# Kernel optimization log

Hardware: AMD Instinct MI355X
Metric: run time of the kernel (lower is better)

## Reference

```python
import jax, jax.numpy as jnp
import numpy as np

FLOW_ITERS = 8
DUAL_ITERS = 8
DUAL_STEP = 0.1
DUAL_MOM = 0.9
GRAPH_LAYERS = 2
BIG = 1e9


def _sparsemax(z, mask):
    # sparsemax along last axis; masked entries already hold -BIG, zeroed by mask after.
    V = z.shape[-1]
    zs = jnp.sort(z, axis=-1)[..., ::-1]
    cum = jnp.cumsum(zs, axis=-1)
    k = jnp.arange(1, V + 1, dtype=z.dtype)
    support = zs * k > (cum - 1.0)
    k_sel = jnp.sum(support.astype(jnp.int32), axis=-1, keepdims=True)
    tau = (jnp.take_along_axis(cum, k_sel - 1, axis=-1) - 1.0) / k_sel.astype(z.dtype)
    return jnp.maximum(z - tau, 0.0) * mask


def _min_cost_flow(props, demands):
    # iterative proportional flow routing: push relu(inflow - demand) along predicted proportions
    def body(flow, _):
        inflow = jnp.sum(flow, axis=1)[..., None]      # [B,V,1] inflow to each node
        adjusted = jax.nn.relu(inflow - demands)       # excess to re-route
        return props * adjusted, None                  # row i scaled by its excess
    flow0 = jnp.zeros_like(props)
    flow, _ = jax.lax.scan(body, flow0, None, length=FLOW_ITERS)
    return flow


def _dual_flow(dual_diff, adj):
    # Nesterov-momentum projected gradient on cost(x)=x^2 minus linear dual term, x>=0 on edges
    def body(carry, _):
        flow, acc = carry
        look = flow - DUAL_MOM * acc
        grad = 2.0 * look - dual_diff                  # d/dx x^2 - dual_diff
        acc = DUAL_MOM * acc + DUAL_STEP * grad
        flow = adj * jax.nn.relu(flow - acc)
        return (flow, acc), None
    z = jnp.zeros_like(dual_diff)
    (flow, _), _ = jax.lax.scan(body, (z, z), None, length=DUAL_ITERS)
    return flow


def setup_inputs():
    key = jax.random.key(0)
    ks = jax.random.split(key, 32)
    B, V, F, E, D, K, H = 8, 1200, 8, 16, 64, 2, 4
    node_features = jax.random.normal(ks[0], (B, V, F), dtype=jnp.float32)
    node_embeddings = jax.random.normal(ks[1], (B, V, E), dtype=jnp.float32)
    d = jax.random.normal(ks[2], (B, V, 1), dtype=jnp.float32)
    demands = d - jnp.mean(d, axis=1, keepdims=True)   # balanced supply/demand per graph
    eye = jnp.eye(V, dtype=jnp.float32)
    adj = (jax.random.uniform(ks[3], (B, V, V)) < (16.0 / V)).astype(jnp.float32) * (1.0 - eye)
    hop2 = jnp.clip(adj @ adj, 0.0, 1.0) * (1.0 - eye)
    neighborhoods = jnp.stack([adj, hop2], axis=0)     # [K,B,V,V] k-hop neighborhoods

    def dense(k, fin, fout):
        return (jax.random.normal(k, (fin, fout), dtype=jnp.float32) / np.sqrt(fin)).astype(jnp.float32)

    return dict(
        node_features=node_features, node_embeddings=node_embeddings,
        demands=demands, adj=adj, neighborhoods=neighborhoods,
        enc_w0=dense(ks[4], E + F, D), enc_b0=jnp.zeros((D,), jnp.float32),
        enc_w1=dense(ks[5], D, D), enc_b1=jnp.zeros((D,), jnp.float32),
        agg_w=(jax.random.normal(ks[6], (K, D, D)) / np.sqrt(D)).astype(jnp.float32),
        agg_b=jnp.zeros((K, D), jnp.float32),
        att_w=(jax.random.normal(ks[7], (H, D, D)) / np.sqrt(D)).astype(jnp.float32),
        att_b=jnp.zeros((H, D), jnp.float32),
        att_v=(jax.random.normal(ks[8], (H, D)) / np.sqrt(D)).astype(jnp.float32),
        gru_wu=dense(ks[9], 2 * D, D), gru_bu=jnp.zeros((D,), jnp.float32),
        gru_wr=dense(ks[10], 2 * D, D), gru_br=jnp.zeros((D,), jnp.float32),
        gru_wc=dense(ks[11], 2 * D, D), gru_bc=jnp.zeros((D,), jnp.float32),
        dec_w0=dense(ks[12], D, D), dec_b0=jnp.zeros((D,), jnp.float32),
        dec_w1=dense(ks[13], D, 1), dec_b1=jnp.zeros((1,), jnp.float32),
        dual_w0=dense(ks[14], D, D), dual_b0=jnp.zeros((D,), jnp.float32),
        dual_w1=dense(ks[15], D, 1), dual_b1=jnp.zeros((1,), jnp.float32),
    )


def reference(node_features, node_embeddings, demands, adj, neighborhoods,
              enc_w0, enc_b0, enc_w1, enc_b1, agg_w, agg_b, att_w, att_b, att_v,
              gru_wu, gru_bu, gru_wr, gru_br, gru_wc, gru_bc,
              dec_w0, dec_b0, dec_w1, dec_b1, dual_w0, dual_b0, dual_w1, dual_b1):
    H = att_w.shape[0]
    # node encoder MLP (tanh hidden, tanh final since activate_final=True)
    x = jnp.concatenate([node_embeddings, node_features], axis=-1)
    enc = jnp.tanh(jnp.tanh(x @ enc_w0 + enc_b0) @ enc_w1 + enc_b1)            # [B,V,D]

    deg = jnp.sum(neighborhoods, axis=-1, keepdims=True)
    nb_norm = neighborhoods / jnp.maximum(deg, 1.0)                            # [K,B,V,V]

    for _ in range(GRAPH_LAYERS):
        # per-hop neighborhood aggregation
        msg = jnp.einsum('kbuv,bvd->kbud', nb_norm, enc)
        agg = jnp.tanh(jnp.einsum('kbud,kde->kbue', msg, agg_w) + agg_b[:, None, None, :])
        # multi-head attention over the K hop levels
        proj = jnp.tanh(jnp.einsum('kbvd,hde->hkbve', agg, att_w) + att_b[:, None, None, None, :])
        scores = jnp.einsum('hkbve,he->hkbv', proj, att_v)
        attn = jax.nn.softmax(scores, axis=1)                                  # softmax over hops
        nxt = jnp.einsum('hkbv,kbvd->bvd', attn, agg) / H                      # mean over heads
        # GRU state update
        xs = jnp.concatenate([nxt, enc], axis=-1)
        u = jax.nn.sigmoid(xs @ gru_wu + gru_bu)
        r = jax.nn.sigmoid(xs @ gru_wr + gru_br)
        c = jnp.tanh(jnp.concatenate([nxt, r * enc], axis=-1) @ gru_wc + gru_bc)
        enc = u * enc + (1.0 - u) * c

    # primal: edge weights -> sparsemax -> min-cost-flow
    pred = (enc @ dec_w0 + dec_b0) @ dec_w1 + dec_b1                           # [B,V,1]
    pred_weights = adj * jnp.transpose(pred, (0, 2, 1))                        # [B,V,V]
    weights = -BIG * (1.0 - adj) + pred_weights
    flow_props = _sparsemax(weights, adj)
    flow = _min_cost_flow(flow_props, demands)
    flow_cost = jnp.sum(flow * flow, axis=(1, 2))                              # square cost

    # dual: potentials -> dual-diff -> dual flow solver
    dual = (enc @ dual_w0 + dual_b0) @ dual_w1 + dual_b1                       # [B,V,1]
    dual_diff = adj * (dual - jnp.transpose(dual, (0, 2, 1)))
    dflow = _dual_flow(dual_diff, adj)
    dual_demand = jnp.sum(dual * demands, axis=(1, 2))
    dual_cost = jnp.sum(dflow * dflow - dual_diff * dflow, axis=(1, 2)) - dual_demand

    return flow_cost - dual_cost                                               # duality-gap loss, [B]
```

## Files before the change

### kernel.cpp

```cpp
#include <hip/hip_runtime.h>

#define BB 8
#define VV 1200
#define DD 64
#define KH 2
#define NH 4
#define CAP 64
#define NB2CAP 384
#define NROW (BB*VV)
#define NKROW (KH*BB*VV)

__device__ __forceinline__ float wredsum(float v) {
#pragma unroll
  for (int o = 32; o > 0; o >>= 1) v += __shfl_xor(v, o, 64);
  return v;
}
__device__ __forceinline__ float gredsum(float v) {
#pragma unroll
  for (int o = 8; o > 0; o >>= 1) v += __shfl_xor(v, o, 64);
  return v;
}

__device__ __forceinline__ float tanh_f(float x) {
  float e = __expf(2.0f * x);
  return 1.0f - 2.0f / (e + 1.0f);
}
__device__ __forceinline__ float sigmoid_f(float x) { return 1.0f / (1.0f + __expf(-x)); }

__device__ __forceinline__ size_t nb_base(int row) {
  return (row < NROW) ? (size_t)row * CAP
                      : (size_t)NROW * CAP + (size_t)(row - NROW) * NB2CAP;
}

__global__ void __launch_bounds__(256) k_pre(
    const float* __restrict__ nb, int* __restrict__ nb_cols, int* __restrict__ nb_cnt,
    const float* __restrict__ emb, const float* __restrict__ feat,
    const float* __restrict__ w0, const float* __restrict__ b0,
    const float* __restrict__ w1, const float* __restrict__ b1,
    float* __restrict__ enc0,
    int* __restrict__ col_cnt, float* __restrict__ out, int out_size) {
  __shared__ float xT[8][25];
  __shared__ float hT[8][65];
  const int nbBlocks = NKROW / 4;
  const int encBlocks = NROW / 8;
  int bid = blockIdx.x;
  int tid = threadIdx.x;
  if (bid < nbBlocks) {
    int wid = tid >> 6, lane = tid & 63;
    int row = bid * 4 + wid;
    const float* nbrow = nb + (size_t)row * VV;
    size_t base = nb_base(row);
    int cap = (row < NROW) ? CAP : NB2CAP;
    unsigned long long ltmask = (lane == 0) ? 0ull : ((1ull << lane) - 1ull);
    int cnt = 0;
    for (int b0_ = 0; b0_ < VV; b0_ += 64) {
      int v = b0_ + lane;
      float val = (v < VV) ? nbrow[v] : 0.0f;
      unsigned long long mask = __ballot(val != 0.0f);
      int off = cnt + __popcll(mask & ltmask);
      if (val != 0.0f && off < cap) nb_cols[base + off] = v;
      cnt += __popcll(mask);
    }
    if (lane == 0) nb_cnt[row] = (cnt > cap) ? cap : cnt;
  } else if (bid < nbBlocks + encBlocks) {
    int tile0 = (bid - nbBlocks) * 8;
    if (tid < 128) { int i = tid >> 4, d = tid & 15; xT[i][d] = emb[(size_t)(tile0 + i) * 16 + d]; }
    else if (tid < 192) { int t = tid - 128; int i = t >> 3, d = t & 7; xT[i][16 + d] = feat[(size_t)(tile0 + i) * 8 + d]; }
    __syncthreads();
    int r = tid >> 5, cg = tid & 31;
    int c0 = cg * 2;
    float a0 = b0[c0], a1 = b0[c0 + 1];
#pragma unroll
    for (int kk = 0; kk < 24; ++kk) {
      float x = xT[r][kk];
      float2 w2 = *(const float2*)(w0 + kk * DD + c0);
      a0 = fmaf(x, w2.x, a0); a1 = fmaf(x, w2.y, a1);
    }
    hT[r][c0] = tanh_f(a0); hT[r][c0 + 1] = tanh_f(a1);
    __syncthreads();
    float g0 = b1[c0], g1 = b1[c0 + 1];
#pragma unroll 16
    for (int kk = 0; kk < DD; ++kk) {
      float x = hT[r][kk];
      float2 w2 = *(const float2*)(w1 + kk * DD + c0);
      g0 = fmaf(x, w2.x, g0); g1 = fmaf(x, w2.y, g1);
    }
    float2 o; o.x = tanh_f(g0); o.y = tanh_f(g1);
    *(float2*)(enc0 + (size_t)(tile0 + r) * DD + c0) = o;
  } else {
    for (int i = tid; i < NROW; i += 256) col_cnt[i] = 0;
    if (tid < out_size) out[tid] = 0.0f;
  }
}

__global__ void __launch_bounds__(256) k_gather(
    const int* __restrict__ nb_cols, const int* __restrict__ nb_cnt,
    const float* __restrict__ encIn, float* __restrict__ msg) {
  int w = threadIdx.x >> 6, lane = threadIdx.x & 63;
  int row = blockIdx.x * 4 + w;
  int k = (row >= NROW) ? 1 : 0;
  int bv = row - k * NROW;
  int b = bv / VV;
  const float4* enc4 = (const float4*)(encIn + (size_t)b * VV * DD);
  const int* cols = nb_cols + nb_base(row);
  int n = nb_cnt[row];
  int sub = lane >> 4, q = lane & 15;
  float ax = 0.0f, ay = 0.0f, az = 0.0f, aw = 0.0f;
  int j = 0;
  int cc0 = 0, cc1 = 0, cc2 = 0, cc3 = 0;
  if (j + 16 <= n) {
    cc0 = cols[j + sub]; cc1 = cols[j + 4 + sub];
    cc2 = cols[j + 8 + sub]; cc3 = cols[j + 12 + sub];
  }
  while (j + 16 <= n) {
    int nj = j + 16;
    int p0 = 0, p1 = 0, p2 = 0, p3 = 0;
    if (nj + 16 <= n) {
      p0 = cols[nj + sub]; p1 = cols[nj + 4 + sub];
      p2 = cols[nj + 8 + sub]; p3 = cols[nj + 12 + sub];
    }
    float4 v0 = enc4[(size_t)cc0 * 16 + q];
    float4 v1 = enc4[(size_t)cc1 * 16 + q];
    float4 v2 = enc4[(size_t)cc2 * 16 + q];
    float4 v3 = enc4[(size_t)cc3 * 16 + q];
    ax += (v0.x + v1.x) + (v2.x + v3.x);
    ay += (v0.y + v1.y) + (v2.y + v3.y);
    az += (v0.z + v1.z) + (v2.z + v3.z);
    aw += (v0.w + v1.w) + (v2.w + v3.w);
    cc0 = p0; cc1 = p1; cc2 = p2; cc3 = p3;
    j = nj;
  }
  for (; j < n; j += 4) {
    int idx = j + sub;
    if (idx < n) {
      float4 v = enc4[(size_t)cols[idx] * 16 + q];
      ax += v.x; ay += v.y; az += v.z; aw += v.w;
    }
  }
#pragma unroll
  for (int o = 16; o < 64; o <<= 1) {
    ax += __shfl_xor(ax, o, 64);
    ay += __shfl_xor(ay, o, 64);
    az += __shfl_xor(az, o, 64);
    aw += __shfl_xor(aw, o, 64);
  }
  if (lane < 16) {
    float inv = 1.0f / fmaxf((float)n, 1.0f);
    float4 r; r.x = ax * inv; r.y = ay * inv; r.z = az * inv; r.w = aw * inv;
    ((float4*)(msg + (size_t)row * DD))[q] = r;
  }
}

__global__ void __launch_bounds__(512) k_aggatt(
    const float* __restrict__ msg,
    const float* __restrict__ agg_w, const float* __restrict__ agg_b,
    const float* __restrict__ att_w, const float* __restrict__ att_b,
    const float* __restrict__ att_v,
    float* __restrict__ agg, float* __restrict__ scores) {
  __shared__ float M[64][65];
  __shared__ float G[64][65];
  int tid = threadIdx.x;
  int tile0 = blockIdx.x * 64;
  int k = (tile0 >= NROW) ? 1 : 0;
  int bv0 = tile0 - k * NROW;
  int rsub = tid >> 4, cg = tid & 15;
  int c0 = cg * 4;
  int r0 = rsub * 2;
#pragma unroll
  for (int rep = 0; rep < 2; ++rep) {
    int idx = rep * 512 + tid; int i = idx >> 4, d4 = idx & 15;
    float4 m4 = *(const float4*)(msg + (size_t)(tile0 + i) * DD + d4 * 4);
    M[i][d4 * 4] = m4.x; M[i][d4 * 4 + 1] = m4.y; M[i][d4 * 4 + 2] = m4.z; M[i][d4 * 4 + 3] = m4.w;
  }
  __syncthreads();
  const float* W = agg_w + (size_t)k * DD * DD;
  float acc[2][4];
#pragma unroll
  for (int i = 0; i < 2; ++i)
#pragma unroll
    for (int j = 0; j < 4; ++j) acc[i][j] = agg_b[k * DD + c0 + j];
#pragma unroll 4
  for (int kk = 0; kk < DD; ++kk) {
    float4 w4 = *(const float4*)(W + kk * DD + c0);
    float x0 = M[r0][kk], x1 = M[r0 + 1][kk];
    acc[0][0] = fmaf(x0, w4.x, acc[0][0]); acc[0][1] = fmaf(x0, w4.y, acc[0][1]);
    acc[0][2] = fmaf(x0, w4.z, acc[0][2]); acc[0][3] = fmaf(x0, w4.w, acc[0][3]);
    acc[1][0] = fmaf(x1, w4.x, acc[1][0]); acc[1][1] = fmaf(x1, w4.y, acc[1][1]);
    acc[1][2] = fmaf(x1, w4.z, acc[1][2]); acc[1][3] = fmaf(x1, w4.w, acc[1][3]);
  }
#pragma unroll
  for (int i = 0; i < 2; ++i) {
    float4 g4;
    g4.x = tanh_f(acc[i][0]); g4.y = tanh_f(acc[i][1]);
    g4.z = tanh_f(acc[i][2]); g4.w = tanh_f(acc[i][3]);
    G[r0 + i][c0] = g4.x; G[r0 + i][c0 + 1] = g4.y; G[r0 + i][c0 + 2] = g4.z; G[r0 + i][c0 + 3] = g4.w;
    *(float4*)(agg + (size_t)(tile0 + r0 + i) * DD + c0) = g4;
  }
  __syncthreads();
#pragma unroll
  for (int h = 0; h < NH; ++h) {
    const float* Wh = att_w + (size_t)h * DD * DD;
    float a2[2][4];
#pragma unroll
    for (int i = 0; i < 2; ++i)
#pragma unroll
      for (int j = 0; j < 4; ++j) a2[i][j] = att_b[h * DD + c0 + j];
#pragma unroll 4
    for (int kk = 0; kk < DD; ++kk) {
      float4 w4 = *(const float4*)(Wh + kk * DD + c0);
      float x0 = G[r0][kk], x1 = G[r0 + 1][kk];
      a2[0][0] = fmaf(x0, w4.x, a2[0][0]); a2[0][1] = fmaf(x0, w4.y, a2[0][1]);
      a2[0][2] = fmaf(x0, w4.z, a2[0][2]); a2[0][3] = fmaf(x0, w4.w, a2[0][3]);
      a2[1][0] = fmaf(x1, w4.x, a2[1][0]); a2[1][1] = fmaf(x1, w4.y, a2[1][1]);
      a2[1][2] = fmaf(x1, w4.z, a2[1][2]); a2[1][3] = fmaf(x1, w4.w, a2[1][3]);
    }
    float4 v4 = *(const float4*)(att_v + h * DD + c0);
#pragma unroll
    for (int i = 0; i < 2; ++i) {
      float p = tanh_f(a2[i][0]) * v4.x + tanh_f(a2[i][1]) * v4.y
              + tanh_f(a2[i][2]) * v4.z + tanh_f(a2[i][3]) * v4.w;
      p = gredsum(p);
      if (cg == 0) scores[(size_t)(h * KH + k) * NROW + bv0 + r0 + i] = p;
    }
  }
}

__global__ void __launch_bounds__(512) k_gru(
    const float* __restrict__ encIn, const float* __restrict__ agg,
    const float* __restrict__ scores,
    const float* __restrict__ wu, const float* __restrict__ bu,
    const float* __restrict__ wr, const float* __restrict__ br,
    const float* __restrict__ wc, const float* __restrict__ bc,
    float* __restrict__ encOut,
    int do_decode,
    const float* __restrict__ dw0, const float* __restrict__ db0,
    const float* __restrict__ dw1, const float* __restrict__ db1,
    const float* __restrict__ uw0, const float* __restrict__ ub0,
    const float* __restrict__ uw1, const float* __restrict__ ub1,
    float* __restrict__ pred, float* __restrict__ dualp) {
  __shared__ float X[64][129];
  __shared__ float EO[64][65];
  int tid = threadIdx.x;
  int tile0 = blockIdx.x * 64;
  int rsub = tid >> 4, cg = tid & 15;
  int c0 = cg * 4;
  int r0 = rsub * 2;
#pragma unroll
  for (int rep = 0; rep < 2; ++rep) {
    int idx = rep * 512 + tid; int i = idx >> 4, d4 = idx & 15;
    int row = tile0 + i;
    float W0 = 0.0f, W1 = 0.0f;
#pragma unroll
    for (int h = 0; h < NH; ++h) {
      float s0 = scores[(size_t)(h * KH + 0) * NROW + row];
      float s1 = scores[(size_t)(h * KH + 1) * NROW + row];
      float m = fmaxf(s0, s1);
      float e0 = __expf(s0 - m), e1 = __expf(s1 - m);
      float inv = 1.0f / (e0 + e1);
      W0 += e0 * inv; W1 += e1 * inv;
    }
    W0 *= 0.25f; W1 *= 0.25f;
    float4 e4 = *(const float4*)(encIn + (size_t)row * DD + d4 * 4);
    float4 a0 = *(const float4*)(agg + (size_t)row * DD + d4 * 4);
    float4 a1 = *(const float4*)(agg + (size_t)(NROW + row) * DD + d4 * 4);
    X[i][d4 * 4]     = W0 * a0.x + W1 * a1.x;
    X[i][d4 * 4 + 1] = W0 * a0.y + W1 * a1.y;
    X[i][d4 * 4 + 2] = W0 * a0.z + W1 * a1.z;
    X[i][d4 * 4 + 3] = W0 * a0.w + W1 * a1.w;
    X[i][64 + d4 * 4]     = e4.x;
    X[i][64 + d4 * 4 + 1] = e4.y;
    X[i][64 + d4 * 4 + 2] = e4.z;
    X[i][64 + d4 * 4 + 3] = e4.w;
  }
  __syncthreads();
  float au[2][4], ar[2][4];
#pragma unroll
  for (int i = 0; i < 2; ++i)
#pragma unroll
    for (int j = 0; j < 4; ++j) { au[i][j] = bu[c0 + j]; ar[i][j] = br[c0 + j]; }
#pragma unroll 4
  for (int kk = 0; kk < 2 * DD; ++kk) {
    float4 u4 = *(const float4*)(wu + kk * DD + c0);
    float4 r4 = *(const float4*)(wr + kk * DD + c0);
    float x0 = X[r0][kk], x1 = X[r0 + 1][kk];
    au[0][0] = fmaf(x0, u4.x, au[0][0]); au[0][1] = fmaf(x0, u4.y, au[0][1]);
    au[0][2] = fmaf(x0, u4.z, au[0][2]); au[0][3] = fmaf(x0, u4.w, au[0][3]);
    au[1][0] = fmaf(x1, u4.x, au[1][0]); au[1][1] = fmaf(x1, u4.y, au[1][1]);
    au[1][2] = fmaf(x1, u4.z, au[1][2]); au[1][3] = fmaf(x1, u4.w, au[1][3]);
    ar[0][0] = fmaf(x0, r4.x, ar[0][0]); ar[0][1] = fmaf(x0, r4.y, ar[0][1]);
    ar[0][2] = fmaf(x0, r4.z, ar[0][2]); ar[0][3] = fmaf(x0, r4.w, ar[0][3]);
    ar[1][0] = fmaf(x1, r4.x, ar[1][0]); ar[1][1] = fmaf(x1, r4.y, ar[1][1]);
    ar[1][2] = fmaf(x1, r4.z, ar[1][2]); ar[1][3] = fmaf(x1, r4.w, ar[1][3]);
  }
  float uu[2][4], encv[2][4];
#pragma unroll
  for (int i = 0; i < 2; ++i)
#pragma unroll
    for (int j = 0; j < 4; ++j) {
      uu[i][j] = sigmoid_f(au[i][j]);
      encv[i][j] = X[r0 + i][64 + c0 + j];
    }
  __syncthreads();
#pragma unroll
  for (int i = 0; i < 2; ++i)
#pragma unroll
    for (int j = 0; j < 4; ++j)
      X[r0 + i][64 + c0 + j] = encv[i][j] * sigmoid_f(ar[i][j]);
  __syncthreads();
  float ac[2][4];
#pragma unroll
  for (int i = 0; i < 2; ++i)
#pragma unroll
    for (int j = 0; j < 4; ++j) ac[i][j] = bc[c0 + j];
#pragma unroll 4
  for (int kk = 0; kk < 2 * DD; ++kk) {
    float4 c4 = *(const float4*)(wc + kk * DD + c0);
    float x0 = X[r0][kk], x1 = X[r0 + 1][kk];
    ac[0][0] = fmaf(x0, c4.x, ac[0][0]); ac[0][1] = fmaf(x0, c4.y, ac[0][1]);
    ac[0][2] = fmaf(x0, c4.z, ac[0][2]); ac[0][3] = fmaf(x0, c4.w, ac[0][3]);
    ac[1][0] = fmaf(x1, c4.x, ac[1][0]); ac[1][1] = fmaf(x1, c4.y, ac[1][1]);
    ac[1][2] = fmaf(x1, c4.z, ac[1][2]); ac[1][3] = fmaf(x1, c4.w, ac[1][3]);
  }
#pragma unroll
  for (int i = 0; i < 2; ++i) {
    float4 e4;
    e4.x = uu[i][0] * encv[i][0] + (1.0f - uu[i][0]) * tanh_f(ac[i][0]);
    e4.y = uu[i][1] * encv[i][1] + (1.0f - uu[i][1]) * tanh_f(ac[i][1]);
    e4.z = uu[i][2] * encv[i][2] + (1.0f - uu[i][2]) * tanh_f(ac[i][2]);
    e4.w = uu[i][3] * encv[i][3] + (1.0f - uu[i][3]) * tanh_f(ac[i][3]);
    *(float4*)(encOut + (size_t)(tile0 + r0 + i) * DD + c0) = e4;
    EO[r0 + i][c0] = e4.x; EO[r0 + i][c0 + 1] = e4.y;
    EO[r0 + i][c0 + 2] = e4.z; EO[r0 + i][c0 + 3] = e4.w;
  }
  if (do_decode) {
    __syncthreads();
    float hd[2][4], hq[2][4];
#pragma unroll
    for (int i = 0; i < 2; ++i)
#pragma unroll
      for (int j = 0; j < 4; ++j) { hd[i][j] = db0[c0 + j]; hq[i][j] = ub0[c0 + j]; }
#pragma unroll 4
    for (int kk = 0; kk < DD; ++kk) {
      float4 d4 = *(const float4*)(dw0 + kk * DD + c0);
      float4 q4 = *(const float4*)(uw0 + kk * DD + c0);
      float x0 = EO[r0][kk], x1 = EO[r0 + 1][kk];
      hd[0][0] = fmaf(x0, d4.x, hd[0][0]); hd[0][1] = fmaf(x0, d4.y, hd[0][1]);
      hd[0][2] = fmaf(x0, d4.z, hd[0][2]); hd[0][3] = fmaf(x0, d4.w, hd[0][3]);
      hd[1][0] = fmaf(x1, d4.x, hd[1][0]); hd[1][1] = fmaf(x1, d4.y, hd[1][1]);
      hd[1][2] = fmaf(x1, d4.z, hd[1][2]); hd[1][3] = fmaf(x1, d4.w, hd[1][3]);
      hq[0][0] = fmaf(x0, q4.x, hq[0][0]); hq[0][1] = fmaf(x0, q4.y, hq[0][1]);
      hq[0][2] = fmaf(x0, q4.z, hq[0][2]); hq[0][3] = fmaf(x0, q4.w, hq[0][3]);
      hq[1][0] = fmaf(x1, q4.x, hq[1][0]); hq[1][1] = fmaf(x1, q4.y, hq[1][1]);
      hq[1][2] = fmaf(x1, q4.z, hq[1][2]); hq[1][3] = fmaf(x1, q4.w, hq[1][3]);
    }
    float4 dv = *(const float4*)(dw1 + c0);
    float4 qv = *(const float4*)(uw1 + c0);
#pragma unroll
    for (int i = 0; i < 2; ++i) {
      float p = hd[i][0] * dv.x + hd[i][1] * dv.y + hd[i][2] * dv.z + hd[i][3] * dv.w;
      float q = hq[i][0] * qv.x + hq[i][1] * qv.y + hq[i][2] * qv.z + hq[i][3] * qv.w;
      p = gredsum(p);
      q = gredsum(q);
      if (cg == 0) {
        pred[tile0 + r0 + i] = p + db1[0];
        dualp[tile0 + r0 + i] = q + ub1[0];
      }
    }
  }
}

__global__ void __launch_bounds__(256) k_primal_dual(
    const int* __restrict__ nb_cols, const int* __restrict__ nb_cnt,
    const float* __restrict__ pred, const float* __restrict__ dualp,
    const float* __restrict__ dem,
    float* __restrict__ rowsum,
    int* __restrict__ col_cnt, int* __restrict__ col_rows, float* __restrict__ col_vals,
    float* __restrict__ out) {
  __shared__ float bacc[BB];
  if (threadIdx.x < BB) bacc[threadIdx.x] = 0.0f;
  __syncthreads();
  int w = threadIdx.x >> 6, lane = threadIdx.x & 63;
  int row = blockIdx.x * 4 + w;
  int b = row / VV;
  int n = nb_cnt[row];
  int c = (lane < n) ? nb_cols[(size_t)row * CAP + lane] : 0;
  const float* predB = pred + (size_t)b * VV;
  const float* dualB = dualp + (size_t)b * VV;
  float z = (lane < n) ? predB[c] : -1e30f;
  float tau = 0.0f;
  if (n > 0) {
    bool in = (lane < n);
    for (int it = 0; it < 64; ++it) {
      float s = wredsum(in ? z : 0.0f);
      int cnt = (int)__popcll(__ballot(in));
      tau = (s - 1.0f) / (float)cnt;
      bool nin = (z > tau);
      if (__ballot(nin) == __ballot(in)) break;
      in = nin;
    }
  }
  float pv = (lane < n) ? fmaxf(z - tau, 0.0f) : 0.0f;
  float s2 = wredsum(pv * pv);
  if (lane == 0) rowsum[row] = s2;
  if (pv > 0.0f) {
    int g = b * VV + c;
    int j = atomicAdd(&col_cnt[g], 1);
    if (j < CAP) {
      col_rows[(size_t)g * CAP + j] = row - b * VV;
      col_vals[(size_t)g * CAP + j] = pv;
    }
  }
  float du = dualp[row];
  float es = 0.0f;
  if (lane < n) {
    float dd = du - dualB[c];
    float f = 0.0f, acm = 0.0f;
#pragma unroll
    for (int t = 0; t < 8; ++t) {
      float look = f - 0.9f * acm;
      float grad = 2.0f * look - dd;
      acm = 0.9f * acm + 0.1f * grad;
      f = fmaxf(f - acm, 0.0f);
    }
    es = f * f - dd * f;
  }
  float contrib = -es;
  if (lane == 0) contrib += du * dem[row];
  float ws_ = wredsum(contrib);
  if (lane == 0) atomicAdd(&bacc[b], ws_);
  __syncthreads();
  if (threadIdx.x < BB) {
    float t = bacc[threadIdx.x];
    if (t != 0.0f) atomicAdd(&out[threadIdx.x], t);
  }
}

__global__ void __launch_bounds__(1024) k_flow(
    const int* __restrict__ col_cnt, const int* __restrict__ col_rows,
    const float* __restrict__ col_vals, const float* __restrict__ dem,
    const float* __restrict__ rowsum, float* __restrict__ out) {
  __shared__ float aS[VV];
  __shared__ float red[16];
  int b = blockIdx.x;
  int tid = threadIdx.x;
  const float* demB = dem + (size_t)b * VV;
  for (int v = tid; v < VV; v += 1024) aS[v] = fmaxf(-demB[v], 0.0f);
  __syncthreads();
  for (int t = 0; t < 7; ++t) {
    float nv0 = 0.0f, nv1 = 0.0f;
    {
      int v = tid;
      if (v < VV) {
        int g = b * VV + v;
        int n = col_cnt[g]; if (n > CAP) n = CAP;
        const int* cr = col_rows + (size_t)g * CAP;
        const float* cv = col_vals + (size_t)g * CAP;
        float acc = 0.0f;
        for (int j = 0; j < n; ++j) acc += cv[j] * aS[cr[j]];
        nv0 = fmaxf(acc - demB[v], 0.0f);
      }
      v = tid + 1024;
      if (v < VV) {
        int g = b * VV + v;
        int n = col_cnt[g]; if (n > CAP) n = CAP;
        const int* cr = col_rows + (size_t)g * CAP;
        const float* cv = col_vals + (size_t)g * CAP;
        float acc = 0.0f;
        for (int j = 0; j < n; ++j) acc += cv[j] * aS[cr[j]];
        nv1 = fmaxf(acc - demB[v], 0.0f);
      }
    }
    __syncthreads();
    if (tid < VV) aS[tid] = nv0;
    if (tid + 1024 < VV) aS[tid + 1024] = nv1;
    __syncthreads();
  }
  float fc = 0.0f;
  for (int v = tid; v < VV; v += 1024) { float a = aS[v]; fc += a * a * rowsum[b * VV + v]; }
  fc = wredsum(fc);
  int wid = tid >> 6, lane = tid & 63;
  if (lane == 0) red[wid] = fc;
  __syncthreads();
  if (tid == 0) {
    float s = 0.0f;
#pragma unroll
    for (int i = 0; i < 16; ++i) s += red[i];
    atomicAdd(&out[b], s);
  }
}

extern "C" void kernel_launch(void* const* d_in, const int* in_sizes, int n_in,
                              void* d_out, int out_size, void* d_ws, size_t ws_size,
                              hipStream_t stream) {
  const float* feat   = (const float*)d_in[0];
  const float* emb    = (const float*)d_in[1];
  const float* dem    = (const float*)d_in[2];
  const float* nb     = (const float*)d_in[4];
  const float* enc_w0 = (const float*)d_in[5];
  const float* enc_b0 = (const float*)d_in[6];
  const float* enc_w1 = (const float*)d_in[7];
  const float* enc_b1 = (const float*)d_in[8];
  const float* agg_w  = (const float*)d_in[9];
  const float* agg_b  = (const float*)d_in[10];
  const float* att_w  = (const float*)d_in[11];
  const float* att_b  = (const float*)d_in[12];
  const float* att_v  = (const float*)d_in[13];
  const float* gru_wu = (const float*)d_in[14];
  const float* gru_bu = (const float*)d_in[15];
  const float* gru_wr = (const float*)d_in[16];
  const float* gru_br = (const float*)d_in[17];
  const float* gru_wc = (const float*)d_in[18];
  const float* gru_bc = (const float*)d_in[19];
  const float* dec_w0 = (const float*)d_in[20];
  const float* dec_b0 = (const float*)d_in[21];
  const float* dec_w1 = (const float*)d_in[22];
  const float* dec_b1 = (const float*)d_in[23];
  const float* dual_w0= (const float*)d_in[24];
  const float* dual_b0= (const float*)d_in[25];
  const float* dual_w1= (const float*)d_in[26];
  const float* dual_b1= (const float*)d_in[27];
  float* out = (float*)d_out;

  float* ws = (float*)d_ws;
  float* enc0     = ws;
  float* enc1     = enc0 + (size_t)NROW * DD;
  float* msg      = enc1 + (size_t)NROW * DD;
  float* aggbuf   = msg + (size_t)NKROW * DD;
  float* scores   = aggbuf + (size_t)NKROW * DD;
  float* pred     = scores + (size_t)NH * KH * NROW;
  float* dualp    = pred + NROW;
  float* rowsum   = dualp + NROW;
  float* col_vals = rowsum + NROW;
  int* col_cnt  = (int*)(col_vals + (size_t)NROW * CAP);
  int* nb_cnt   = col_cnt + NROW;
  int* col_rows = nb_cnt + NKROW;
  int* nb_cols  = col_rows + (size_t)NROW * CAP;

  (void)in_sizes; (void)n_in; (void)ws_size;

  k_pre<<<NKROW / 4 + NROW / 8 + 1, 256, 0, stream>>>(
      nb, nb_cols, nb_cnt, emb, feat, enc_w0, enc_b0, enc_w1, enc_b1, enc0,
      col_cnt, out, out_size);

  const float* encIn = enc0;
  float* encOut = enc1;
  for (int l = 0; l < 2; ++l) {
    k_gather<<<NKROW / 4, 256, 0, stream>>>(nb_cols, nb_cnt, encIn, msg);
    k_aggatt<<<NKROW / 64, 512, 0, stream>>>(msg, agg_w, agg_b, att_w, att_b, att_v,
                                             aggbuf, scores);
    k_gru<<<NROW / 64, 512, 0, stream>>>(encIn, aggbuf, scores,
                                         gru_wu, gru_bu, gru_wr, gru_br, gru_wc, gru_bc,
                                         encOut,
                                         (l == 1) ? 1 : 0,
                                         dec_w0, dec_b0, dec_w1, dec_b1,
                                         dual_w0, dual_b0, dual_w1, dual_b1, pred, dualp);
    const float* t = encIn; encIn = encOut; encOut = (float*)t;
  }

  k_primal_dual<<<NROW / 4, 256, 0, stream>>>(nb_cols, nb_cnt, pred, dualp, dem,
                                              rowsum, col_cnt, col_rows, col_vals, out);
  k_flow<<<BB, 1024, 0, stream>>>(col_cnt, col_rows, col_vals, dem, rowsum, out);
}
```

Measured before the change: 547.7 us.

## Store node encodings as bf16 and vectorize neighbor-mask compaction loads

The intermediate node encodings passed between layers are stored as packed bf16 pairs instead of fp32, which halves the bytes moved by the neighbor gather and the GRU encoding reads. The gather kernel unpacks them to fp32 for accumulation. Separately, the neighbor-mask compaction in the preprocessing kernel now reads float4 per lane and uses four ballots, cutting the number of loop iterations. The price is reduced precision in the recurrent state, which may move results against the tolerance.

New measurement: 546.5 us. No clear change (-0.2%).

```diff
diff --git a/kernel.cpp b/kernel.cpp
--- a/kernel.cpp
+++ b/kernel.cpp
@@ -27,6 +27,15 @@
 }
 __device__ __forceinline__ float sigmoid_f(float x) { return 1.0f / (1.0f + __expf(-x)); }
 
+__device__ __forceinline__ unsigned pack_bf16x2(float a, float b) {
+  unsigned ua = __float_as_uint(a), ub = __float_as_uint(b);
+  ua = (ua + 0x7fffu + ((ua >> 16) & 1u)) >> 16;
+  ub = (ub + 0x7fffu + ((ub >> 16) & 1u)) & 0xffff0000u;
+  return ua | ub;
+}
+__device__ __forceinline__ float bf_lo(unsigned u) { return __uint_as_float(u << 16); }
+__device__ __forceinline__ float bf_hi(unsigned u) { return __uint_as_float(u & 0xffff0000u); }
+
 __device__ __forceinline__ size_t nb_base(int row) {
   return (row < NROW) ? (size_t)row * CAP
                       : (size_t)NROW * CAP + (size_t)(row - NROW) * NB2CAP;
@@ -37,7 +46,7 @@
     const float* __restrict__ emb, const float* __restrict__ feat,
     const float* __restrict__ w0, const float* __restrict__ b0,
     const float* __restrict__ w1, const float* __restrict__ b1,
-    float* __restrict__ enc0,
+    unsigned* __restrict__ enc0,
     int* __restrict__ col_cnt, float* __restrict__ out, int out_size) {
   __shared__ float xT[8][25];
   __shared__ float hT[8][65];
@@ -48,18 +57,30 @@
   if (bid < nbBlocks) {
     int wid = tid >> 6, lane = tid & 63;
     int row = bid * 4 + wid;
-    const float* nbrow = nb + (size_t)row * VV;
+    const float4* nb4 = (const float4*)(nb + (size_t)row * VV);
     size_t base = nb_base(row);
     int cap = (row < NROW) ? CAP : NB2CAP;
     unsigned long long ltmask = (lane == 0) ? 0ull : ((1ull << lane) - 1ull);
     int cnt = 0;
-    for (int b0_ = 0; b0_ < VV; b0_ += 64) {
-      int v = b0_ + lane;
-      float val = (v < VV) ? nbrow[v] : 0.0f;
-      unsigned long long mask = __ballot(val != 0.0f);
-      int off = cnt + __popcll(mask & ltmask);
-      if (val != 0.0f && off < cap) nb_cols[base + off] = v;
-      cnt += __popcll(mask);
+    for (int b0_ = 0; b0_ < VV; b0_ += 256) {
+      int vi = b0_ + lane * 4;
+      float4 v4 = {0.0f, 0.0f, 0.0f, 0.0f};
+      if (vi < VV) v4 = nb4[(b0_ >> 2) + lane];
+      int nz0 = (v4.x != 0.0f), nz1 = (v4.y != 0.0f), nz2 = (v4.z != 0.0f), nz3 = (v4.w != 0.0f);
+      unsigned long long m0 = __ballot(nz0 != 0);
+      unsigned long long m1 = __ballot(nz1 != 0);
+      unsigned long long m2 = __ballot(nz2 != 0);
+      unsigned long long m3 = __ballot(nz3 != 0);
+      int off = cnt + __popcll(m0 & ltmask) + __popcll(m1 & ltmask)
+                    + __popcll(m2 & ltmask) + __popcll(m3 & ltmask);
+      if (nz0 && off < cap) nb_cols[base + off] = vi;
+      off += nz0;
+      if (nz1 && off < cap) nb_cols[base + off] = vi + 1;
+      off += nz1;
+      if (nz2 && off < cap) nb_cols[base + off] = vi + 2;
+      off += nz2;
+      if (nz3 && off < cap) nb_cols[base + off] = vi + 3;
+      cnt += __popcll(m0) + __popcll(m1) + __popcll(m2) + __popcll(m3);
     }
     if (lane == 0) nb_cnt[row] = (cnt > cap) ? cap : cnt;
   } else if (bid < nbBlocks + encBlocks) {
@@ -85,8 +106,7 @@
       float2 w2 = *(const float2*)(w1 + kk * DD + c0);
       g0 = fmaf(x, w2.x, g0); g1 = fmaf(x, w2.y, g1);
     }
-    float2 o; o.x = tanh_f(g0); o.y = tanh_f(g1);
-    *(float2*)(enc0 + (size_t)(tile0 + r) * DD + c0) = o;
+    enc0[(size_t)(tile0 + r) * 32 + cg] = pack_bf16x2(tanh_f(g0), tanh_f(g1));
   } else {
     for (int i = tid; i < NROW; i += 256) col_cnt[i] = 0;
     if (tid < out_size) out[tid] = 0.0f;
@@ -95,13 +115,13 @@
 
 __global__ void __launch_bounds__(256) k_gather(
     const int* __restrict__ nb_cols, const int* __restrict__ nb_cnt,
-    const float* __restrict__ encIn, float* __restrict__ msg) {
+    const unsigned* __restrict__ encIn, float* __restrict__ msg) {
   int w = threadIdx.x >> 6, lane = threadIdx.x & 63;
   int row = blockIdx.x * 4 + w;
   int k = (row >= NROW) ? 1 : 0;
   int bv = row - k * NROW;
   int b = bv / VV;
-  const float4* enc4 = (const float4*)(encIn + (size_t)b * VV * DD);
+  const uint2* encU = (const uint2*)(encIn + (size_t)b * VV * 32);
   const int* cols = nb_cols + nb_base(row);
   int n = nb_cnt[row];
   int sub = lane >> 4, q = lane & 15;
@@ -119,22 +139,22 @@
       p0 = cols[nj + sub]; p1 = cols[nj + 4 + sub];
       p2 = cols[nj + 8 + sub]; p3 = cols[nj + 12 + sub];
     }
-    float4 v0 = enc4[(size_t)cc0 * 16 + q];
-    float4 v1 = enc4[(size_t)cc1 * 16 + q];
-    float4 v2 = enc4[(size_t)cc2 * 16 + q];
-    float4 v3 = enc4[(size_t)cc3 * 16 + q];
-    ax += (v0.x + v1.x) + (v2.x + v3.x);
-    ay += (v0.y + v1.y) + (v2.y + v3.y);
-    az += (v0.z + v1.z) + (v2.z + v3.z);
-    aw += (v0.w + v1.w) + (v2.w + v3.w);
+    uint2 u0 = encU[(size_t)cc0 * 16 + q];
+    uint2 u1 = encU[(size_t)cc1 * 16 + q];
+    uint2 u2 = encU[(size_t)cc2 * 16 + q];
+    uint2 u3 = encU[(size_t)cc3 * 16 + q];
+    ax += (bf_lo(u0.x) + bf_lo(u1.x)) + (bf_lo(u2.x) + bf_lo(u3.x));
+    ay += (bf_hi(u0.x) + bf_hi(u1.x)) + (bf_hi(u2.x) + bf_hi(u3.x));
+    az += (bf_lo(u0.y) + bf_lo(u1.y)) + (bf_lo(u2.y) + bf_lo(u3.y));
+    aw += (bf_hi(u0.y) + bf_hi(u1.y)) + (bf_hi(u2.y) + bf_hi(u3.y));
     cc0 = p0; cc1 = p1; cc2 = p2; cc3 = p3;
     j = nj;
   }
   for (; j < n; j += 4) {
     int idx = j + sub;
     if (idx < n) {
-      float4 v = enc4[(size_t)cols[idx] * 16 + q];
-      ax += v.x; ay += v.y; az += v.z; aw += v.w;
+      uint2 u = encU[(size_t)cols[idx] * 16 + q];
+      ax += bf_lo(u.x); ay += bf_hi(u.x); az += bf_lo(u.y); aw += bf_hi(u.y);
     }
   }
 #pragma unroll
@@ -226,12 +246,12 @@
 }
 
 __global__ void __launch_bounds__(512) k_gru(
-    const float* __restrict__ encIn, const float* __restrict__ agg,
+    const unsigned* __restrict__ encIn, const float* __restrict__ agg,
     const float* __restrict__ scores,
     const float* __restrict__ wu, const float* __restrict__ bu,
     const float* __restrict__ wr, const float* __restrict__ br,
     const float* __restrict__ wc, const float* __restrict__ bc,
-    float* __restrict__ encOut,
+    unsigned* __restrict__ encOut,
     int do_decode,
     const float* __restrict__ dw0, const float* __restrict__ db0,
     const float* __restrict__ dw1, const float* __restrict__ db1,
@@ -260,17 +280,17 @@
       W0 += e0 * inv; W1 += e1 * inv;
     }
     W0 *= 0.25f; W1 *= 0.25f;
-    float4 e4 = *(const float4*)(encIn + (size_t)row * DD + d4 * 4);
+    uint2 eu = ((const uint2*)encIn)[(size_t)row * 16 + d4];
     float4 a0 = *(const float4*)(agg + (size_t)row * DD + d4 * 4);
     float4 a1 = *(const float4*)(agg + (size_t)(NROW + row) * DD + d4 * 4);
     X[i][d4 * 4]     = W0 * a0.x + W1 * a1.x;
     X[i][d4 * 4 + 1] = W0 * a0.y + W1 * a1.y;
     X[i][d4 * 4 + 2] = W0 * a0.z + W1 * a1.z;
     X[i][d4 * 4 + 3] = W0 * a0.w + W1 * a1.w;
-    X[i][64 + d4 * 4]     = e4.x;
-    X[i][64 + d4 * 4 + 1] = e4.y;
-    X[i][64 + d4 * 4 + 2] = e4.z;
-    X[i][64 + d4 * 4 + 3] = e4.w;
+    X[i][64 + d4 * 4]     = bf_lo(eu.x);
+    X[i][64 + d4 * 4 + 1] = bf_hi(eu.x);
+    X[i][64 + d4 * 4 + 2] = bf_lo(eu.y);
+    X[i][64 + d4 * 4 + 3] = bf_hi(eu.y);
   }
   __syncthreads();
   float au[2][4], ar[2][4];
@@ -328,7 +348,8 @@
     e4.y = uu[i][1] * encv[i][1] + (1.0f - uu[i][1]) * tanh_f(ac[i][1]);
     e4.z = uu[i][2] * encv[i][2] + (1.0f - uu[i][2]) * tanh_f(ac[i][2]);
     e4.w = uu[i][3] * encv[i][3] + (1.0f - uu[i][3]) * tanh_f(ac[i][3]);
-    *(float4*)(encOut + (size_t)(tile0 + r0 + i) * DD + c0) = e4;
+    uint2 pk; pk.x = pack_bf16x2(e4.x, e4.y); pk.y = pack_bf16x2(e4.z, e4.w);
+    ((uint2*)encOut)[(size_t)(tile0 + r0 + i) * 16 + cg] = pk;
     EO[r0 + i][c0] = e4.x; EO[r0 + i][c0 + 1] = e4.y;
     EO[r0 + i][c0 + 2] = e4.z; EO[r0 + i][c0 + 3] = e4.w;
   }
@@ -521,10 +542,9 @@
   const float* dual_b1= (const float*)d_in[27];
   float* out = (float*)d_out;
 
-  float* ws = (float*)d_ws;
-  float* enc0     = ws;
-  float* enc1     = enc0 + (size_t)NROW * DD;
-  float* msg      = enc1 + (size_t)NROW * DD;
+  unsigned* enc0 = (unsigned*)d_ws;
+  unsigned* enc1 = enc0 + (size_t)NROW * 32;
+  float* msg      = (float*)(enc1 + (size_t)NROW * 32);
   float* aggbuf   = msg + (size_t)NKROW * DD;
   float* scores   = aggbuf + (size_t)NKROW * DD;
   float* pred     = scores + (size_t)NH * KH * NROW;
@@ -542,8 +562,8 @@
       nb, nb_cols, nb_cnt, emb, feat, enc_w0, enc_b0, enc_w1, enc_b1, enc0,
       col_cnt, out, out_size);
 
-  const float* encIn = enc0;
-  float* encOut = enc1;
+  const unsigned* encIn = enc0;
+  unsigned* encOut = enc1;
   for (int l = 0; l < 2; ++l) {
     k_gather<<<NKROW / 4, 256, 0, stream>>>(nb_cols, nb_cnt, encIn, msg);
     k_aggatt<<<NKROW / 64, 512, 0, stream>>>(msg, agg_w, agg_b, att_w, att_b, att_v,
@@ -554,7 +574,7 @@
                                          (l == 1) ? 1 : 0,
                                          dec_w0, dec_b0, dec_w1, dec_b1,
                                          dual_w0, dual_b0, dual_w1, dual_b1, pred, dualp);
-    const float* t = encIn; encIn = encOut; encOut = (float*)t;
+    const unsigned* t = encIn; encIn = encOut; encOut = (unsigned*)t;
   }
 
   k_primal_dual<<<NROW / 4, 256, 0, stream>>>(nb_cols, nb_cnt, pred, dualp, dem,
```
